# Optimization experiments

Hardware: AMD Instinct MI355X
Metric: run time of the kernel (lower is better)

The kernel has to match this reference:

```python
import jax, jax.numpy as jnp
import numpy as np

N_EMBD = 1024
N_HEAD = 16
B, T = 8, 1024
EPS = 1e-5


def setup_inputs() -> dict:
    key = jax.random.key(0)
    ks = jax.random.split(key, 12)
    C = N_EMBD
    s_in = 1.0 / np.sqrt(C)
    s_ff = 1.0 / np.sqrt(4 * C)
    inp = {
        "x": jax.random.normal(ks[0], (B, T, C), dtype=jnp.float32),
        "mask": jnp.tril(jnp.ones((T, T), dtype=jnp.int32))[None, None, :, :],
        "ln1_w": jnp.ones((C,), jnp.float32),
        "ln1_b": jnp.zeros((C,), jnp.float32),
        "ln2_w": jnp.ones((C,), jnp.float32),
        "ln2_b": jnp.zeros((C,), jnp.float32),
        "wq": jax.random.normal(ks[1], (C, C), jnp.float32) * s_in,
        "bq": jnp.zeros((C,), jnp.float32),
        "wk": jax.random.normal(ks[2], (C, C), jnp.float32) * s_in,
        "bk": jnp.zeros((C,), jnp.float32),
        "wv": jax.random.normal(ks[3], (C, C), jnp.float32) * s_in,
        "bv": jnp.zeros((C,), jnp.float32),
        "wo": jax.random.normal(ks[4], (C, C), jnp.float32) * s_in,
        "bo": jnp.zeros((C,), jnp.float32),
        "w1": jax.random.normal(ks[5], (C, 4 * C), jnp.float32) * s_in,
        "b1": jnp.zeros((4 * C,), jnp.float32),
        "w2": jax.random.normal(ks[6], (4 * C, C), jnp.float32) * s_ff,
        "b2": jnp.zeros((C,), jnp.float32),
    }
    return inp


def _layer_norm(x, w, b):
    mu = jnp.mean(x, axis=-1, keepdims=True)
    var = jnp.mean(jnp.square(x - mu), axis=-1, keepdims=True)
    return (x - mu) * jax.lax.rsqrt(var + EPS) * w + b


def reference(x, mask, ln1_w, ln1_b, ln2_w, ln2_b,
              wq, bq, wk, bk, wv, bv, wo, bo, w1, b1, w2, b2):
    Bx, Tx, C = x.shape
    H = N_HEAD
    d = C // H
    h = _layer_norm(x, ln1_w, ln1_b)
    q = (h @ wq + bq).reshape(Bx, Tx, H, d)
    k = (h @ wk + bk).reshape(Bx, Tx, H, d)
    v = (h @ wv + bv).reshape(Bx, Tx, H, d)
    # [B,H,Tq,Tk] scores, scaled by sqrt(head_dim)
    scores = jnp.einsum('bqhd,bkhd->bhqk', q, k) / jnp.sqrt(jnp.float32(d))
    scores = jnp.where(mask == 0, -jnp.inf, scores)
    attn = jax.nn.softmax(scores, axis=-1)
    ctx = jnp.einsum('bhqk,bkhd->bqhd', attn, v).reshape(Bx, Tx, C)
    x = x + (ctx @ wo + bo)
    h2 = _layer_norm(x, ln2_w, ln2_b)
    ff = jax.nn.gelu(h2 @ w1 + b1, approximate=False) @ w2 + b2
    return x + ff
```

## Files before the change

kernel.cpp:

```cpp
#include <hip/hip_runtime.h>
#include <hip/hip_bf16.h>
#include <math.h>


#define DEVI __device__ __forceinline__

typedef __attribute__((ext_vector_type(4))) float floatx4;
typedef __attribute__((ext_vector_type(8))) short shortx8;

DEVI ushort f2b(float f) {
    __hip_bfloat16 h = __float2bfloat16(f);
    return __builtin_bit_cast(ushort, h);
}

DEVI void gl_lds16(const ushort* g, ushort* l) {
    __builtin_amdgcn_global_load_lds(
        (const __attribute__((address_space(1))) void*)g,
        (__attribute__((address_space(3))) void*)l, 16, 0, 0);
}

DEVI float gelu_f(float v) {
    const float u0 = 0.7978845608f * v * (1.0f + 0.044715f * v * v);
    const float u  = fminf(fmaxf(u0, -15.0f), 15.0f);
    const float e  = exp2f(u * 2.885390082f);
    const float th = 1.0f - 2.0f / (e + 1.0f);
    return 0.5f * v * (1.0f + th);
}

__global__ void transp_all(const float* __restrict__ s0, const float* __restrict__ s1,
                           const float* __restrict__ s2, const float* __restrict__ s3,
                           const float* __restrict__ s4, const float* __restrict__ s5,
                           ushort* __restrict__ d0, ushort* __restrict__ d1,
                           ushort* __restrict__ d2, ushort* __restrict__ d3,
                           ushort* __restrict__ d4, ushort* __restrict__ d5) {
    __shared__ float tile[32][33];
    const int i = blockIdx.x;
    const float* src; ushort* dst; int R, C, bx, by;
    if (i < 4096) {
        const int m = i >> 10, t = i & 1023;
        src = (m == 0) ? s0 : (m == 1) ? s1 : (m == 2) ? s2 : s3;
        dst = (m == 0) ? d0 : (m == 1) ? d1 : (m == 2) ? d2 : d3;
        R = 1024; C = 1024; bx = t & 31; by = t >> 5;
    } else if (i < 8192) {
        const int t = i - 4096;
        src = s4; dst = d4; R = 1024; C = 4096;
        bx = t & 127; by = t >> 7;
    } else {
        const int t = i - 8192;
        src = s5; dst = d5; R = 4096; C = 1024;
        bx = t & 31; by = t >> 5;
    }
    const int c0 = bx * 32, r0 = by * 32;
    const int tx = threadIdx.x, ty = threadIdx.y;
#pragma unroll
    for (int p = 0; p < 32; p += 8)
        tile[ty + p][tx] = src[(size_t)(r0 + ty + p) * C + c0 + tx];
    __syncthreads();
#pragma unroll
    for (int p = 0; p < 32; p += 8)
        dst[(size_t)(c0 + ty + p) * R + r0 + tx] = f2b(tile[tx][ty + p]);
}

__global__ __launch_bounds__(256)
void ln_kernel(const float* __restrict__ x, const float* __restrict__ w,
               const float* __restrict__ b, ushort* __restrict__ out) {
    __shared__ float red[8];
    const int m = blockIdx.x;
    const int tid = threadIdx.x;
    const float4 xv = *(const float4*)&x[(size_t)m * 1024 + tid * 4];
    float s  = xv.x + xv.y + xv.z + xv.w;
    float s2 = xv.x * xv.x + xv.y * xv.y + xv.z * xv.z + xv.w * xv.w;
#pragma unroll
    for (int o = 32; o >= 1; o >>= 1) {
        s  += __shfl_xor(s, o, 64);
        s2 += __shfl_xor(s2, o, 64);
    }
    const int wv_ = tid >> 6;
    if ((tid & 63) == 0) { red[wv_] = s; red[4 + wv_] = s2; }
    __syncthreads();
    s  = red[0] + red[1] + red[2] + red[3];
    s2 = red[4] + red[5] + red[6] + red[7];
    const float mu   = s * (1.0f / 1024.0f);
    const float var  = s2 * (1.0f / 1024.0f) - mu * mu;
    const float rstd = rsqrtf(var + 1e-5f);
    const float4 wv = *(const float4*)&w[tid * 4];
    const float4 bv = *(const float4*)&b[tid * 4];
    ushort o4[4];
    o4[0] = f2b((xv.x - mu) * rstd * wv.x + bv.x);
    o4[1] = f2b((xv.y - mu) * rstd * wv.y + bv.y);
    o4[2] = f2b((xv.z - mu) * rstd * wv.z + bv.z);
    o4[3] = f2b((xv.w - mu) * rstd * wv.w + bv.w);
    *(uint2*)&out[(size_t)m * 1024 + tid * 4] = *(uint2*)o4;
}

template <int MODE>
__global__ __launch_bounds__(256, MODE == 1 ? 3 : 4)
void gemm97(const ushort* __restrict__ A, const ushort* __restrict__ Bt,
            const float* __restrict__ biasQ, const float* __restrict__ biasK,
            const float* __restrict__ biasV,
            void* __restrict__ out, void* __restrict__ out2, void* __restrict__ out3,
            int N, int K) {
    __shared__ __align__(128) ushort lds[MODE == 1 ? 21504 : 18432];

    const int tid  = threadIdx.x;
    const int lane = tid & 63;
    const int w    = tid >> 6;
    const int wr   = w >> 1;
    const int wc   = w & 1;

    int bx = blockIdx.x, by = blockIdx.y;
    {
        const int nwg = gridDim.x * gridDim.y;
        if ((nwg & 7) == 0) {
            const int flat = by * gridDim.x + bx;
            const int cpx  = nwg >> 3;
            const int wg   = (flat & 7) * cpx + (flat >> 3);
            bx = wg % gridDim.x;
            by = wg / gridDim.x;
        }
    }
    const int m0 = by * 128;
    const int n0 = bx * 128;

    floatx4 acc[4][4] = {};

    const int lr3 = lane >> 3;
    const int sc  = (lane & 7) ^ lr3;
    const ushort* pA = A  + (size_t)(m0 + w * 32 + lr3) * K + sc * 8;
    const ushort* pB = Bt + (size_t)(n0 + w * 32 + lr3) * K + sc * 8;
    ushort* sAd = lds + w * 2048;
    ushort* sBd = lds + 8192 + w * 2048;
    const size_t k8 = (size_t)8 * K, k16 = (size_t)16 * K, k24 = (size_t)24 * K;

    const int c0f = (lane >> 4) ^ (lane & 7);
    const int aIdx = (wr * 64 + (lane & 15)) * 64 + c0f * 8;
    const int bIdx = (wc * 64 + (lane & 15)) * 64 + c0f * 8;
    const ushort* ar0 = lds + aIdx;
    const ushort* ar1 = lds + (aIdx ^ 32);
    const ushort* br0 = lds + 8192 + bIdx;
    const ushort* br1 = lds + 8192 + (bIdx ^ 32);

    for (int k0 = 0; k0 < K; k0 += 64) {
        __syncthreads();
        gl_lds16(pA + k0,       sAd);
        gl_lds16(pA + k8  + k0, sAd + 512);
        gl_lds16(pA + k16 + k0, sAd + 1024);
        gl_lds16(pA + k24 + k0, sAd + 1536);
        gl_lds16(pB + k0,       sBd);
        gl_lds16(pB + k8  + k0, sBd + 512);
        gl_lds16(pB + k16 + k0, sBd + 1024);
        gl_lds16(pB + k24 + k0, sBd + 1536);
        asm volatile("s_waitcnt vmcnt(0)" ::: "memory");
        __syncthreads();

        shortx8 af[4][2], bf[4][2];
#pragma unroll
        for (int mi = 0; mi < 4; ++mi) {
            af[mi][0] = *(const shortx8*)&ar0[mi * 1024];
            af[mi][1] = *(const shortx8*)&ar1[mi * 1024];
        }
#pragma unroll
        for (int ni = 0; ni < 4; ++ni) {
            bf[ni][0] = *(const shortx8*)&br0[ni * 1024];
            bf[ni][1] = *(const shortx8*)&br1[ni * 1024];
        }
#pragma unroll
        for (int mi = 0; mi < 4; ++mi)
#pragma unroll
            for (int ni = 0; ni < 4; ++ni) {
                acc[mi][ni] = __builtin_amdgcn_mfma_f32_16x16x32_bf16(
                    af[mi][0], bf[ni][0], acc[mi][ni], 0, 0, 0);
                acc[mi][ni] = __builtin_amdgcn_mfma_f32_16x16x32_bf16(
                    af[mi][1], bf[ni][1], acc[mi][ni], 0, 0, 0);
            }
    }
    __syncthreads();

    const int colL  = wc * 64 + (lane & 15);
    const int rbase = wr * 64 + ((lane >> 4) << 2);

    if constexpr (MODE == 3) {
        float bvals[4];
#pragma unroll
        for (int ni = 0; ni < 4; ++ni) bvals[ni] = biasQ[n0 + colL + ni * 16];
        ushort* T = lds;
#pragma unroll
        for (int mi = 0; mi < 4; ++mi)
#pragma unroll
        for (int ni = 0; ni < 4; ++ni) {
            const int t0 = rbase + mi * 16;
#pragma unroll
            for (int r = 0; r < 4; ++r)
                T[(t0 + r) * 136 + colL + ni * 16] =
                    f2b(gelu_f(acc[mi][ni][r] + bvals[ni]));
        }
        __syncthreads();
        ushort* o = (ushort*)out;
#pragma unroll
        for (int it = 0; it < 8; ++it) {
            const int idx = it * 256 + tid;
            const int row = idx >> 4, ch = idx & 15;
            const uint4 vv = *(const uint4*)&T[row * 136 + ch * 8];
            *(uint4*)&o[(size_t)(m0 + row) * N + n0 + ch * 8] = vv;
        }
    }

    if constexpr (MODE == 1) {
        const int mat   = n0 >> 10;
        const int bb    = m0 >> 10;
        const int tbase = m0 & 1023;
        if (mat < 2) {
            const float* bp = (mat == 0) ? biasQ : biasK;
            ushort* dst = (mat == 0) ? (ushort*)out : (ushort*)out2;
            const int cb = n0 & 1023;
            float bvals[4];
#pragma unroll
            for (int ni = 0; ni < 4; ++ni) bvals[ni] = bp[cb + colL + ni * 16];
            ushort* T = lds;
#pragma unroll
            for (int mi = 0; mi < 4; ++mi)
#pragma unroll
            for (int ni = 0; ni < 4; ++ni) {
                const int t0 = rbase + mi * 16;
#pragma unroll
                for (int r = 0; r < 4; ++r)
                    T[(t0 + r) * 136 + colL + ni * 16] =
                        f2b(acc[mi][ni][r] + bvals[ni]);
            }
            __syncthreads();
#pragma unroll
            for (int it = 0; it < 8; ++it) {
                const int idx = it * 256 + tid;
                const int row = idx >> 4, ch = idx & 15;
                const uint4 vv = *(const uint4*)&T[row * 136 + ch * 8];
                *(uint4*)&dst[(size_t)(m0 + row) * 1024 + cb + ch * 8] = vv;
            }
        } else {
            const int vb = n0 - 2048;
            ushort* T = lds;
            ushort* Vt = (ushort*)out3;
#pragma unroll
            for (int ni = 0; ni < 4; ++ni) {
                const float bv = biasV[vb + colL + ni * 16];
#pragma unroll
                for (int mi = 0; mi < 4; ++mi) {
                    const int t0 = rbase + mi * 16;
#pragma unroll
                    for (int r = 0; r < 4; ++r)
                        T[(colL + ni * 16) * 136 + t0 + r] =
                            f2b(acc[mi][ni][r] + bv);
                }
            }
            __syncthreads();
#pragma unroll
            for (int it = 0; it < 8; ++it) {
                const int idx = it * 256 + tid;
                const int dim = idx >> 4, ch = idx & 15;
                const uint4 vv = *(const uint4*)&T[dim * 136 + ch * 8];
                const int d  = vb + dim;
                const int hh = d >> 6, dl = d & 63;
                *(uint4*)&Vt[((size_t)(bb * 16 + hh) * 64 + dl) * 1024 + tbase + ch * 8] = vv;
            }
        }
    }
}

__global__ __launch_bounds__(256, 4)
void gemm97r(const ushort* __restrict__ A, const ushort* __restrict__ Bt,
             const float* __restrict__ bias, float* __restrict__ out,
             const float* __restrict__ resid, int N, int K) {
    __shared__ __align__(128) ushort lds[18432];

    const int tid  = threadIdx.x;
    const int lane = tid & 63;
    const int w    = tid >> 6;
    const int wr   = w >> 1;
    const int wc   = w & 1;

    int bx = blockIdx.x, by = blockIdx.y;
    {
        const int nwg = gridDim.x * gridDim.y;
        if ((nwg & 7) == 0) {
            const int flat = by * gridDim.x + bx;
            const int cpx  = nwg >> 3;
            const int wg   = (flat & 7) * cpx + (flat >> 3);
            bx = wg % gridDim.x;
            by = wg / gridDim.x;
        }
    }
    const int m0 = by * 128;
    const int n0 = bx * 128;

    floatx4 acc[4][4] = {};

    const int lr3 = lane >> 3;
    const int sc  = (lane & 7) ^ lr3;
    const ushort* pA = A  + (size_t)(m0 + w * 32 + lr3) * K + sc * 8;
    const ushort* pB = Bt + (size_t)(n0 + w * 32 + lr3) * K + sc * 8;
    ushort* sAd = lds + w * 2048;
    ushort* sBd = lds + 8192 + w * 2048;
    const size_t k8 = (size_t)8 * K, k16 = (size_t)16 * K, k24 = (size_t)24 * K;

    const int c0f = (lane >> 4) ^ (lane & 7);
    const int aIdx = (wr * 64 + (lane & 15)) * 64 + c0f * 8;
    const int bIdx = (wc * 64 + (lane & 15)) * 64 + c0f * 8;
    const ushort* ar0 = lds + aIdx;
    const ushort* ar1 = lds + (aIdx ^ 32);
    const ushort* br0 = lds + 8192 + bIdx;
    const ushort* br1 = lds + 8192 + (bIdx ^ 32);

    for (int k0 = 0; k0 < K; k0 += 64) {
        __syncthreads();
        gl_lds16(pA + k0,       sAd);
        gl_lds16(pA + k8  + k0, sAd + 512);
        gl_lds16(pA + k16 + k0, sAd + 1024);
        gl_lds16(pA + k24 + k0, sAd + 1536);
        gl_lds16(pB + k0,       sBd);
        gl_lds16(pB + k8  + k0, sBd + 512);
        gl_lds16(pB + k16 + k0, sBd + 1024);
        gl_lds16(pB + k24 + k0, sBd + 1536);
        asm volatile("s_waitcnt vmcnt(0)" ::: "memory");
        __syncthreads();

        shortx8 af[4][2], bf[4][2];
#pragma unroll
        for (int mi = 0; mi < 4; ++mi) {
            af[mi][0] = *(const shortx8*)&ar0[mi * 1024];
            af[mi][1] = *(const shortx8*)&ar1[mi * 1024];
        }
#pragma unroll
        for (int ni = 0; ni < 4; ++ni) {
            bf[ni][0] = *(const shortx8*)&br0[ni * 1024];
            bf[ni][1] = *(const shortx8*)&br1[ni * 1024];
        }
#pragma unroll
        for (int mi = 0; mi < 4; ++mi)
#pragma unroll
            for (int ni = 0; ni < 4; ++ni) {
                acc[mi][ni] = __builtin_amdgcn_mfma_f32_16x16x32_bf16(
                    af[mi][0], bf[ni][0], acc[mi][ni], 0, 0, 0);
                acc[mi][ni] = __builtin_amdgcn_mfma_f32_16x16x32_bf16(
                    af[mi][1], bf[ni][1], acc[mi][ni], 0, 0, 0);
            }
    }
    __syncthreads();

    const int colL  = wc * 64 + (lane & 15);
    const int rbase = wr * 64 + ((lane >> 4) << 2);
    float bvals[4];
#pragma unroll
    for (int ni = 0; ni < 4; ++ni) bvals[ni] = bias[n0 + colL + ni * 16];
    float* T = (float*)lds;
    float* o = (float*)out;
#pragma unroll
    for (int half = 0; half < 2; ++half) {
        if (wr == half) {
#pragma unroll
            for (int mi = 0; mi < 4; ++mi)
#pragma unroll
            for (int ni = 0; ni < 4; ++ni) {
                const int t0 = mi * 16 + ((lane >> 4) << 2);
#pragma unroll
                for (int r = 0; r < 4; ++r)
                    T[(t0 + r) * 132 + colL + ni * 16] =
                        acc[mi][ni][r] + bvals[ni];
            }
        }
        __syncthreads();
#pragma unroll
        for (int it = 0; it < 8; ++it) {
            const int idx = it * 256 + tid;
            const int row = idx >> 5, ch = idx & 31;
            float4 tv = *(const float4*)&T[row * 132 + ch * 4];
            const size_t go = (size_t)(m0 + half * 64 + row) * N + n0 + ch * 4;
            const float4 rv = *(const float4*)&resid[go];
            tv.x += rv.x; tv.y += rv.y; tv.z += rv.z; tv.w += rv.w;
            *(float4*)&o[go] = tv;
        }
        __syncthreads();
    }
}

__global__ __launch_bounds__(256)
void attn_kernel(const ushort* __restrict__ Q, const ushort* __restrict__ Kk,
                 const ushort* __restrict__ Vt, ushort* __restrict__ ctx) {
    __shared__ ushort sK[64 * 64];
    __shared__ ushort sV[64 * 64];
    __shared__ ushort sP[4][16 * 72];

    const int tid  = threadIdx.x;
    const int lane = tid & 63;
    const int wave = tid >> 6;
    const int quad = lane >> 4;
    const int l15  = lane & 15;

    const int qb = 15 - (blockIdx.x >> 7);
    const int bh = blockIdx.x & 127;
    const size_t vbase = (size_t)bh << 16;
    const int bb = bh >> 4, h = bh & 15;

    const int lrow = lane >> 3;
    const int scb  = (lane & 7) ^ lrow;
    const ushort* Kg = Kk + ((size_t)bb * 1024 + wave * 8 + lrow) * 1024 + h * 64 + scb * 8;
    const ushort* Vg = Vt + vbase + (size_t)(wave * 8 + lrow) * 1024 + scb * 8;

    const int qrow = bb * 1024 + qb * 64 + wave * 16 + l15;
    const shortx8 qf0 = *(const shortx8*)&Q[(size_t)qrow * 1024 + h * 64 + quad * 8];
    const shortx8 qf1 = *(const shortx8*)&Q[(size_t)qrow * 1024 + h * 64 + 32 + quad * 8];

    const float SC = 0.125f * 1.44269504f;

    float mstate[4], lstate[4];
    floatx4 oacc[4] = {};
#pragma unroll
    for (int r = 0; r < 4; ++r) { mstate[r] = -__builtin_inff(); lstate[r] = 0.0f; }

    for (int kt = 0; kt <= qb; ++kt) {
        __syncthreads();
#pragma unroll
        for (int p = 0; p < 2; ++p) {
            gl_lds16(Kg + (size_t)kt * 65536 + (size_t)p * 32768,
                     sK + (p * 32 + wave * 8) * 64);
            gl_lds16(Vg + (size_t)kt * 64 + (size_t)p * 32 * 1024,
                     sV + (p * 32 + wave * 8) * 64);
        }
        __syncthreads();

        floatx4 s[4];
#pragma unroll
        for (int nt = 0; nt < 4; ++nt) {
            const int r = nt * 16 + l15;
            const int c0 = quad ^ (r & 7);
            const int c1 = (4 + quad) ^ (r & 7);
            const shortx8 kf0 = *(const shortx8*)&sK[r * 64 + c0 * 8];
            const shortx8 kf1 = *(const shortx8*)&sK[r * 64 + c1 * 8];
            floatx4 z = {};
            z = __builtin_amdgcn_mfma_f32_16x16x32_bf16(qf0, kf0, z, 0, 0, 0);
            z = __builtin_amdgcn_mfma_f32_16x16x32_bf16(qf1, kf1, z, 0, 0, 0);
            s[nt] = z;
        }
#pragma unroll
        for (int nt = 0; nt < 4; ++nt)
#pragma unroll
            for (int r = 0; r < 4; ++r) {
                float sv = s[nt][r] * SC;
                if (kt == qb) {
                    const int col = nt * 16 + l15;
                    const int row = wave * 16 + quad * 4 + r;
                    if (col > row) sv = -__builtin_inff();
                }
                s[nt][r] = sv;
            }
        float mnew[4], alpha[4];
#pragma unroll
        for (int r = 0; r < 4; ++r) {
            float mt = fmaxf(fmaxf(s[0][r], s[1][r]), fmaxf(s[2][r], s[3][r]));
#pragma unroll
            for (int o = 8; o >= 1; o >>= 1) mt = fmaxf(mt, __shfl_xor(mt, o, 64));
            mnew[r]  = fmaxf(mstate[r], mt);
            alpha[r] = exp2f(mstate[r] - mnew[r]);
            mstate[r] = mnew[r];
        }
#pragma unroll
        for (int r = 0; r < 4; ++r) {
            float rs = 0.0f;
#pragma unroll
            for (int nt = 0; nt < 4; ++nt) {
                const float p = exp2f(s[nt][r] - mnew[r]);
                s[nt][r] = p;
                rs += p;
            }
#pragma unroll
            for (int o = 8; o >= 1; o >>= 1) rs += __shfl_xor(rs, o, 64);
            lstate[r] = alpha[r] * lstate[r] + rs;
#pragma unroll
            for (int dt = 0; dt < 4; ++dt) oacc[dt][r] *= alpha[r];
        }
#pragma unroll
        for (int nt = 0; nt < 4; ++nt)
#pragma unroll
            for (int r = 0; r < 4; ++r)
                sP[wave][(quad * 4 + r) * 72 + nt * 16 + l15] = f2b(s[nt][r]);
        __asm__ volatile("s_waitcnt lgkmcnt(0)" ::: "memory");
        const shortx8 pf0 = *(const shortx8*)&sP[wave][l15 * 72 + quad * 8];
        const shortx8 pf1 = *(const shortx8*)&sP[wave][l15 * 72 + 32 + quad * 8];
#pragma unroll
        for (int dt = 0; dt < 4; ++dt) {
            const int r = dt * 16 + l15;
            const int c0 = quad ^ (r & 7);
            const int c1 = (4 + quad) ^ (r & 7);
            const shortx8 v0 = *(const shortx8*)&sV[r * 64 + c0 * 8];
            const shortx8 v1 = *(const shortx8*)&sV[r * 64 + c1 * 8];
            oacc[dt] = __builtin_amdgcn_mfma_f32_16x16x32_bf16(pf0, v0, oacc[dt], 0, 0, 0);
            oacc[dt] = __builtin_amdgcn_mfma_f32_16x16x32_bf16(pf1, v1, oacc[dt], 0, 0, 0);
        }
    }
#pragma unroll
    for (int dt = 0; dt < 4; ++dt)
#pragma unroll
        for (int r = 0; r < 4; ++r) {
            const int t = qb * 64 + wave * 16 + quad * 4 + r;
            const int dim = dt * 16 + l15;
            const float v = oacc[dt][r] / lstate[r];
            ctx[(size_t)(bb * 1024 + t) * 1024 + h * 64 + dim] = f2b(v);
        }
}

extern "C" void kernel_launch(void* const* d_in, const int* in_sizes, int n_in,
                              void* d_out, int out_size, void* d_ws, size_t ws_size,
                              hipStream_t stream) {
    const float* x    = (const float*)d_in[0];
    const float* ln1w = (const float*)d_in[2];
    const float* ln1b = (const float*)d_in[3];
    const float* ln2w = (const float*)d_in[4];
    const float* ln2b = (const float*)d_in[5];
    const float* wq   = (const float*)d_in[6];
    const float* bq   = (const float*)d_in[7];
    const float* wk   = (const float*)d_in[8];
    const float* bk   = (const float*)d_in[9];
    const float* wv   = (const float*)d_in[10];
    const float* bv   = (const float*)d_in[11];
    const float* wo   = (const float*)d_in[12];
    const float* bo   = (const float*)d_in[13];
    const float* w1   = (const float*)d_in[14];
    const float* b1   = (const float*)d_in[15];
    const float* w2   = (const float*)d_in[16];
    const float* b2   = (const float*)d_in[17];

    char* ws = (char*)d_ws;
    const size_t MB = 1024 * 1024;
    ushort* WQKVT = (ushort*)(ws + 0 * MB);
    ushort* WOT   = (ushort*)(ws + 6 * MB);
    ushort* W1T   = (ushort*)(ws + 8 * MB);
    ushort* W2T   = (ushort*)(ws + 16 * MB);
    ushort* H1    = (ushort*)(ws + 24 * MB);
    ushort* H2    = H1;
    ushort* Qb    = (ushort*)(ws + 40 * MB);
    ushort* Kb    = (ushort*)(ws + 56 * MB);
    ushort* Vbt   = (ushort*)(ws + 72 * MB);
    ushort* FF1   = (ushort*)(ws + 40 * MB);
    ushort* CTX   = (ushort*)(ws + 104 * MB);

    float* xout = (float*)d_out;

    transp_all<<<12288, dim3(32, 8), 0, stream>>>(
        wq, wk, wv, wo, w1, w2,
        WQKVT, WQKVT + 1024 * 1024, WQKVT + 2048 * 1024, WOT, W1T, W2T);

    ln_kernel<<<8192, 256, 0, stream>>>(x, ln1w, ln1b, H1);

    gemm97<1><<<dim3(24, 64), 256, 0, stream>>>(H1, WQKVT, bq, bk, bv,
                                                Qb, Kb, Vbt, 3072, 1024);

    attn_kernel<<<2048, 256, 0, stream>>>(Qb, Kb, Vbt, CTX);

    gemm97r<<<dim3(8, 64), 256, 0, stream>>>(CTX, WOT, bo, xout, x, 1024, 1024);

    ln_kernel<<<8192, 256, 0, stream>>>(xout, ln2w, ln2b, H2);

    gemm97<3><<<dim3(32, 64), 256, 0, stream>>>(H2, W1T, b1, nullptr, nullptr,
                                                FF1, nullptr, nullptr, 4096, 1024);

    gemm97r<<<dim3(8, 64), 256, 0, stream>>>(FF1, W2T, b2, xout, xout, 1024, 4096);

    (void)in_sizes; (void)n_in; (void)out_size; (void)ws_size;
}
```

Before: 475.3 us.

## Retile QKV GEMM to 256x128 with 512 threads and narrow residual GEMMs to 128x64

Measured after the change: 470.7 us. Within noise of the previous version (-1.0%).

```diff
diff --git a/kernel.cpp b/kernel.cpp
--- a/kernel.cpp
+++ b/kernel.cpp
@@ -93,14 +93,13 @@
     *(uint2*)&out[(size_t)m * 1024 + tid * 4] = *(uint2*)o4;
 }
 
-template <int MODE>
-__global__ __launch_bounds__(256, MODE == 1 ? 3 : 4)
-void gemm97(const ushort* __restrict__ A, const ushort* __restrict__ Bt,
+__global__ __launch_bounds__(512, 4)
+void gemmW1(const ushort* __restrict__ A, const ushort* __restrict__ Bt,
             const float* __restrict__ biasQ, const float* __restrict__ biasK,
             const float* __restrict__ biasV,
             void* __restrict__ out, void* __restrict__ out2, void* __restrict__ out3,
             int N, int K) {
-    __shared__ __align__(128) ushort lds[MODE == 1 ? 21504 : 18432];
+    __shared__ __align__(128) ushort lds[24576];
 
     const int tid  = threadIdx.x;
     const int lane = tid & 63;
@@ -119,6 +118,160 @@
             by = wg / gridDim.x;
         }
     }
+    const int m0 = by * 256;
+    const int n0 = bx * 128;
+
+    floatx4 acc[4][4] = {};
+
+    const int lr3 = lane >> 3;
+    const int sc  = (lane & 7) ^ lr3;
+    const ushort* pA = A  + (size_t)(m0 + w * 32 + lr3) * K + sc * 8;
+    const ushort* pB = Bt + (size_t)(n0 + w * 16 + lr3) * K + sc * 8;
+    ushort* sAd = lds + w * 2048;
+    ushort* sBd = lds + 16384 + w * 1024;
+    const size_t k8 = (size_t)8 * K, k16 = (size_t)16 * K, k24 = (size_t)24 * K;
+
+    const int c0f  = (lane >> 4) ^ (lane & 7);
+    const int aIdx = (wr * 64 + (lane & 15)) * 64 + c0f * 8;
+    const int bIdx = (wc * 64 + (lane & 15)) * 64 + c0f * 8;
+    const ushort* ar0 = lds + aIdx;
+    const ushort* ar1 = lds + (aIdx ^ 32);
+    const ushort* br0 = lds + 16384 + bIdx;
+    const ushort* br1 = lds + 16384 + (bIdx ^ 32);
+
+    for (int k0 = 0; k0 < K; k0 += 64) {
+        __syncthreads();
+        gl_lds16(pA + k0,       sAd);
+        gl_lds16(pA + k8  + k0, sAd + 512);
+        gl_lds16(pA + k16 + k0, sAd + 1024);
+        gl_lds16(pA + k24 + k0, sAd + 1536);
+        gl_lds16(pB + k0,       sBd);
+        gl_lds16(pB + k8  + k0, sBd + 512);
+        asm volatile("s_waitcnt vmcnt(0)" ::: "memory");
+        __syncthreads();
+
+        shortx8 af[4][2], bf[4][2];
+#pragma unroll
+        for (int mi = 0; mi < 4; ++mi) {
+            af[mi][0] = *(const shortx8*)&ar0[mi * 1024];
+            af[mi][1] = *(const shortx8*)&ar1[mi * 1024];
+        }
+#pragma unroll
+        for (int ni = 0; ni < 4; ++ni) {
+            bf[ni][0] = *(const shortx8*)&br0[ni * 1024];
+            bf[ni][1] = *(const shortx8*)&br1[ni * 1024];
+        }
+#pragma unroll
+        for (int mi = 0; mi < 4; ++mi)
+#pragma unroll
+            for (int ni = 0; ni < 4; ++ni) {
+                acc[mi][ni] = __builtin_amdgcn_mfma_f32_16x16x32_bf16(
+                    af[mi][0], bf[ni][0], acc[mi][ni], 0, 0, 0);
+                acc[mi][ni] = __builtin_amdgcn_mfma_f32_16x16x32_bf16(
+                    af[mi][1], bf[ni][1], acc[mi][ni], 0, 0, 0);
+            }
+    }
+    __syncthreads();
+
+    const int colL  = wc * 64 + (lane & 15);
+    const int rbase = (wr & 1) * 64 + ((lane >> 4) << 2);
+    const int mqme  = wr >> 1;
+
+    const int mat   = n0 >> 10;
+    const int bb    = m0 >> 10;
+    const int tbase = m0 & 1023;
+    if (mat < 2) {
+        const float* bp = (mat == 0) ? biasQ : biasK;
+        ushort* dst = (mat == 0) ? (ushort*)out : (ushort*)out2;
+        const int cb = n0 & 1023;
+        float bvals[4];
+#pragma unroll
+        for (int ni = 0; ni < 4; ++ni) bvals[ni] = bp[cb + colL + ni * 16];
+        ushort* T = lds;
+#pragma unroll
+        for (int mq = 0; mq < 2; ++mq) {
+            if (mqme == mq) {
+#pragma unroll
+                for (int mi = 0; mi < 4; ++mi)
+#pragma unroll
+                for (int ni = 0; ni < 4; ++ni) {
+                    const int t0 = rbase + mi * 16;
+#pragma unroll
+                    for (int r = 0; r < 4; ++r)
+                        T[(t0 + r) * 136 + colL + ni * 16] =
+                            f2b(acc[mi][ni][r] + bvals[ni]);
+                }
+            }
+            __syncthreads();
+#pragma unroll
+            for (int it = 0; it < 4; ++it) {
+                const int idx = it * 512 + tid;
+                const int row = idx >> 4, ch = idx & 15;
+                const uint4 vv = *(const uint4*)&T[row * 136 + ch * 8];
+                *(uint4*)&dst[(size_t)(m0 + mq * 128 + row) * 1024 + cb + ch * 8] = vv;
+            }
+            __syncthreads();
+        }
+    } else {
+        const int vb = n0 - 2048;
+        ushort* T = lds;
+        ushort* Vt = (ushort*)out3;
+        float bvals[4];
+#pragma unroll
+        for (int ni = 0; ni < 4; ++ni) bvals[ni] = biasV[vb + colL + ni * 16];
+#pragma unroll
+        for (int mq = 0; mq < 2; ++mq) {
+            if (mqme == mq) {
+#pragma unroll
+                for (int ni = 0; ni < 4; ++ni)
+#pragma unroll
+                for (int mi = 0; mi < 4; ++mi) {
+                    const int t0 = rbase + mi * 16;
+#pragma unroll
+                    for (int r = 0; r < 4; ++r)
+                        T[(colL + ni * 16) * 136 + t0 + r] =
+                            f2b(acc[mi][ni][r] + bvals[ni]);
+                }
+            }
+            __syncthreads();
+#pragma unroll
+            for (int it = 0; it < 4; ++it) {
+                const int idx = it * 512 + tid;
+                const int dim = idx >> 4, ch = idx & 15;
+                const uint4 vv = *(const uint4*)&T[dim * 136 + ch * 8];
+                const int d  = vb + dim;
+                const int hh = d >> 6, dl = d & 63;
+                *(uint4*)&Vt[((size_t)(bb * 16 + hh) * 64 + dl) * 1024
+                             + tbase + mq * 128 + ch * 8] = vv;
+            }
+            __syncthreads();
+        }
+    }
+}
+
+__global__ __launch_bounds__(256, 4)
+void gemm97g(const ushort* __restrict__ A, const ushort* __restrict__ Bt,
+             const float* __restrict__ bias, ushort* __restrict__ out,
+             int N, int K) {
+    __shared__ __align__(128) ushort lds[18432];
+
+    const int tid  = threadIdx.x;
+    const int lane = tid & 63;
+    const int w    = tid >> 6;
+    const int wr   = w >> 1;
+    const int wc   = w & 1;
+
+    int bx = blockIdx.x, by = blockIdx.y;
+    {
+        const int nwg = gridDim.x * gridDim.y;
+        if ((nwg & 7) == 0) {
+            const int flat = by * gridDim.x + bx;
+            const int cpx  = nwg >> 3;
+            const int wg   = (flat & 7) * cpx + (flat >> 3);
+            bx = wg % gridDim.x;
+            by = wg / gridDim.x;
+        }
+    }
     const int m0 = by * 128;
     const int n0 = bx * 128;
 
@@ -178,90 +331,27 @@
 
     const int colL  = wc * 64 + (lane & 15);
     const int rbase = wr * 64 + ((lane >> 4) << 2);
-
-    if constexpr (MODE == 3) {
-        float bvals[4];
-#pragma unroll
-        for (int ni = 0; ni < 4; ++ni) bvals[ni] = biasQ[n0 + colL + ni * 16];
-        ushort* T = lds;
-#pragma unroll
-        for (int mi = 0; mi < 4; ++mi)
-#pragma unroll
-        for (int ni = 0; ni < 4; ++ni) {
-            const int t0 = rbase + mi * 16;
-#pragma unroll
-            for (int r = 0; r < 4; ++r)
-                T[(t0 + r) * 136 + colL + ni * 16] =
-                    f2b(gelu_f(acc[mi][ni][r] + bvals[ni]));
-        }
-        __syncthreads();
-        ushort* o = (ushort*)out;
-#pragma unroll
-        for (int it = 0; it < 8; ++it) {
-            const int idx = it * 256 + tid;
-            const int row = idx >> 4, ch = idx & 15;
-            const uint4 vv = *(const uint4*)&T[row * 136 + ch * 8];
-            *(uint4*)&o[(size_t)(m0 + row) * N + n0 + ch * 8] = vv;
-        }
-    }
-
-    if constexpr (MODE == 1) {
-        const int mat   = n0 >> 10;
-        const int bb    = m0 >> 10;
-        const int tbase = m0 & 1023;
-        if (mat < 2) {
-            const float* bp = (mat == 0) ? biasQ : biasK;
-            ushort* dst = (mat == 0) ? (ushort*)out : (ushort*)out2;
-            const int cb = n0 & 1023;
-            float bvals[4];
-#pragma unroll
-            for (int ni = 0; ni < 4; ++ni) bvals[ni] = bp[cb + colL + ni * 16];
-            ushort* T = lds;
-#pragma unroll
-            for (int mi = 0; mi < 4; ++mi)
-#pragma unroll
-            for (int ni = 0; ni < 4; ++ni) {
-                const int t0 = rbase + mi * 16;
-#pragma unroll
-                for (int r = 0; r < 4; ++r)
-                    T[(t0 + r) * 136 + colL + ni * 16] =
-                        f2b(acc[mi][ni][r] + bvals[ni]);
-            }
-            __syncthreads();
-#pragma unroll
-            for (int it = 0; it < 8; ++it) {
-                const int idx = it * 256 + tid;
-                const int row = idx >> 4, ch = idx & 15;
-                const uint4 vv = *(const uint4*)&T[row * 136 + ch * 8];
-                *(uint4*)&dst[(size_t)(m0 + row) * 1024 + cb + ch * 8] = vv;
-            }
-        } else {
-            const int vb = n0 - 2048;
-            ushort* T = lds;
-            ushort* Vt = (ushort*)out3;
-#pragma unroll
-            for (int ni = 0; ni < 4; ++ni) {
-                const float bv = biasV[vb + colL + ni * 16];
-#pragma unroll
-                for (int mi = 0; mi < 4; ++mi) {
-                    const int t0 = rbase + mi * 16;
-#pragma unroll
-                    for (int r = 0; r < 4; ++r)
-                        T[(colL + ni * 16) * 136 + t0 + r] =
-                            f2b(acc[mi][ni][r] + bv);
-                }
-            }
-            __syncthreads();
-#pragma unroll
-            for (int it = 0; it < 8; ++it) {
-                const int idx = it * 256 + tid;
-                const int dim = idx >> 4, ch = idx & 15;
-                const uint4 vv = *(const uint4*)&T[dim * 136 + ch * 8];
-                const int d  = vb + dim;
-                const int hh = d >> 6, dl = d & 63;
-                *(uint4*)&Vt[((size_t)(bb * 16 + hh) * 64 + dl) * 1024 + tbase + ch * 8] = vv;
-            }
-        }
+    float bvals[4];
+#pragma unroll
+    for (int ni = 0; ni < 4; ++ni) bvals[ni] = bias[n0 + colL + ni * 16];
+    ushort* T = lds;
+#pragma unroll
+    for (int mi = 0; mi < 4; ++mi)
+#pragma unroll
+    for (int ni = 0; ni < 4; ++ni) {
+        const int t0 = rbase + mi * 16;
+#pragma unroll
+        for (int r = 0; r < 4; ++r)
+            T[(t0 + r) * 136 + colL + ni * 16] =
+                f2b(gelu_f(acc[mi][ni][r] + bvals[ni]));
+    }
+    __syncthreads();
+#pragma unroll
+    for (int it = 0; it < 8; ++it) {
+        const int idx = it * 256 + tid;
+        const int row = idx >> 4, ch = idx & 15;
+        const uint4 vv = *(const uint4*)&T[row * 136 + ch * 8];
+        *(uint4*)&out[(size_t)(m0 + row) * N + n0 + ch * 8] = vv;
     }
 }
 
@@ -269,13 +359,11 @@
 void gemm97r(const ushort* __restrict__ A, const ushort* __restrict__ Bt,
              const float* __restrict__ bias, float* __restrict__ out,
              const float* __restrict__ resid, int N, int K) {
-    __shared__ __align__(128) ushort lds[18432];
+    __shared__ __align__(128) ushort lds[12288];
 
     const int tid  = threadIdx.x;
     const int lane = tid & 63;
     const int w    = tid >> 6;
-    const int wr   = w >> 1;
-    const int wc   = w & 1;
 
     int bx = blockIdx.x, by = blockIdx.y;
     {
@@ -289,21 +377,21 @@
         }
     }
     const int m0 = by * 128;
-    const int n0 = bx * 128;
-
-    floatx4 acc[4][4] = {};
+    const int n0 = bx * 64;
+
+    floatx4 acc[2][4] = {};
 
     const int lr3 = lane >> 3;
     const int sc  = (lane & 7) ^ lr3;
     const ushort* pA = A  + (size_t)(m0 + w * 32 + lr3) * K + sc * 8;
-    const ushort* pB = Bt + (size_t)(n0 + w * 32 + lr3) * K + sc * 8;
+    const ushort* pB = Bt + (size_t)(n0 + w * 16 + lr3) * K + sc * 8;
     ushort* sAd = lds + w * 2048;
-    ushort* sBd = lds + 8192 + w * 2048;
+    ushort* sBd = lds + 8192 + w * 1024;
     const size_t k8 = (size_t)8 * K, k16 = (size_t)16 * K, k24 = (size_t)24 * K;
 
-    const int c0f = (lane >> 4) ^ (lane & 7);
-    const int aIdx = (wr * 64 + (lane & 15)) * 64 + c0f * 8;
-    const int bIdx = (wc * 64 + (lane & 15)) * 64 + c0f * 8;
+    const int c0f  = (lane >> 4) ^ (lane & 7);
+    const int aIdx = (w * 32 + (lane & 15)) * 64 + c0f * 8;
+    const int bIdx = (lane & 15) * 64 + c0f * 8;
     const ushort* ar0 = lds + aIdx;
     const ushort* ar1 = lds + (aIdx ^ 32);
     const ushort* br0 = lds + 8192 + bIdx;
@@ -317,14 +405,12 @@
         gl_lds16(pA + k24 + k0, sAd + 1536);
         gl_lds16(pB + k0,       sBd);
         gl_lds16(pB + k8  + k0, sBd + 512);
-        gl_lds16(pB + k16 + k0, sBd + 1024);
-        gl_lds16(pB + k24 + k0, sBd + 1536);
         asm volatile("s_waitcnt vmcnt(0)" ::: "memory");
         __syncthreads();
 
-        shortx8 af[4][2], bf[4][2];
-#pragma unroll
-        for (int mi = 0; mi < 4; ++mi) {
+        shortx8 af[2][2], bf[4][2];
+#pragma unroll
+        for (int mi = 0; mi < 2; ++mi) {
             af[mi][0] = *(const shortx8*)&ar0[mi * 1024];
             af[mi][1] = *(const shortx8*)&ar1[mi * 1024];
         }
@@ -334,7 +420,7 @@
             bf[ni][1] = *(const shortx8*)&br1[ni * 1024];
         }
 #pragma unroll
-        for (int mi = 0; mi < 4; ++mi)
+        for (int mi = 0; mi < 2; ++mi)
 #pragma unroll
             for (int ni = 0; ni < 4; ++ni) {
                 acc[mi][ni] = __builtin_amdgcn_mfma_f32_16x16x32_bf16(
@@ -345,8 +431,7 @@
     }
     __syncthreads();
 
-    const int colL  = wc * 64 + (lane & 15);
-    const int rbase = wr * 64 + ((lane >> 4) << 2);
+    const int colL = lane & 15;
     float bvals[4];
 #pragma unroll
     for (int ni = 0; ni < 4; ++ni) bvals[ni] = bias[n0 + colL + ni * 16];
@@ -354,24 +439,25 @@
     float* o = (float*)out;
 #pragma unroll
     for (int half = 0; half < 2; ++half) {
-        if (wr == half) {
-#pragma unroll
-            for (int mi = 0; mi < 4; ++mi)
+        if ((w >> 1) == half) {
+            const int rb = (w & 1) * 32 + ((lane >> 4) << 2);
+#pragma unroll
+            for (int mi = 0; mi < 2; ++mi)
 #pragma unroll
             for (int ni = 0; ni < 4; ++ni) {
-                const int t0 = mi * 16 + ((lane >> 4) << 2);
+                const int t0 = rb + mi * 16;
 #pragma unroll
                 for (int r = 0; r < 4; ++r)
-                    T[(t0 + r) * 132 + colL + ni * 16] =
+                    T[(t0 + r) * 68 + colL + ni * 16] =
                         acc[mi][ni][r] + bvals[ni];
             }
         }
         __syncthreads();
 #pragma unroll
-        for (int it = 0; it < 8; ++it) {
+        for (int it = 0; it < 4; ++it) {
             const int idx = it * 256 + tid;
-            const int row = idx >> 5, ch = idx & 31;
-            float4 tv = *(const float4*)&T[row * 132 + ch * 4];
+            const int row = idx >> 4, ch = idx & 15;
+            float4 tv = *(const float4*)&T[row * 68 + ch * 4];
             const size_t go = (size_t)(m0 + half * 64 + row) * N + n0 + ch * 4;
             const float4 rv = *(const float4*)&resid[go];
             tv.x += rv.x; tv.y += rv.y; tv.z += rv.z; tv.w += rv.w;
@@ -549,19 +635,18 @@
 
     ln_kernel<<<8192, 256, 0, stream>>>(x, ln1w, ln1b, H1);
 
-    gemm97<1><<<dim3(24, 64), 256, 0, stream>>>(H1, WQKVT, bq, bk, bv,
-                                                Qb, Kb, Vbt, 3072, 1024);
+    gemmW1<<<dim3(24, 32), 512, 0, stream>>>(H1, WQKVT, bq, bk, bv,
+                                             Qb, Kb, Vbt, 3072, 1024);
 
     attn_kernel<<<2048, 256, 0, stream>>>(Qb, Kb, Vbt, CTX);
 
-    gemm97r<<<dim3(8, 64), 256, 0, stream>>>(CTX, WOT, bo, xout, x, 1024, 1024);
+    gemm97r<<<dim3(16, 64), 256, 0, stream>>>(CTX, WOT, bo, xout, x, 1024, 1024);
 
     ln_kernel<<<8192, 256, 0, stream>>>(xout, ln2w, ln2b, H2);
 
-    gemm97<3><<<dim3(32, 64), 256, 0, stream>>>(H2, W1T, b1, nullptr, nullptr,
-                                                FF1, nullptr, nullptr, 4096, 1024);
-
-    gemm97r<<<dim3(8, 64), 256, 0, stream>>>(FF1, W2T, b2, xout, xout, 1024, 4096);
+    gemm97g<<<dim3(32, 64), 256, 0, stream>>>(H2, W1T, b1, FF1, 4096, 1024);
+
+    gemm97r<<<dim3(16, 64), 256, 0, stream>>>(FF1, W2T, b2, xout, xout, 1024, 4096);
 
     (void)in_sizes; (void)n_in; (void)out_size; (void)ws_size;
 }
```
